# Performance work log

Measured on AMD Instinct MI355X. Metric: run time of the kernel, lower is better.

## Reference

```python
import jax, jax.numpy as jnp
import numpy as np


def setup_inputs() -> dict:
    key = jax.random.key(0)
    kq, kk, kv, kb = jax.random.split(key, 4)
    B, H, S, D = 4, 16, 1024, 64
    return {
        "query": jax.random.normal(kq, (B, H, S, D), dtype=jnp.float32),
        "key": jax.random.normal(kk, (B, H, S, D), dtype=jnp.float32),
        "value": jax.random.normal(kv, (B, H, S, D), dtype=jnp.float32),
        "bias_mask": jax.random.normal(kb, (1, 1, S, S), dtype=jnp.float32),
    }


def reference(query, key, value, bias_mask):
    d_k = query.shape[-1]
    scale = 1.0 / jnp.sqrt(jnp.asarray(d_k, dtype=query.dtype))
    # scores: [B, H, Sq, Sk]
    scores = jnp.einsum("bhqd,bhkd->bhqk", query, key) * scale
    scores = scores + bias_mask
    attn_weights = jax.nn.softmax(scores, axis=-1)
    output = jnp.einsum("bhqk,bhkd->bhqd", attn_weights, value)
    return (output, attn_weights)
```

## Files before the change

### kernel.cpp

```cpp
#include <hip/hip_runtime.h>

constexpr int SEQ = 1024;
constexpr int DH  = 64;
constexpr int QR  = 32;
constexpr int KT  = 128;
constexpr int NKT = SEQ / KT;
constexpr int KS  = 72;
constexpr int VS  = 136;
constexpr int PS  = 136;

constexpr int BUF = 26112;
constexpr int SPOFF = 17408;

typedef __bf16 bf16x8 __attribute__((ext_vector_type(8)));
typedef __bf16 bf16x4 __attribute__((ext_vector_type(4)));
typedef float  f32x4  __attribute__((ext_vector_type(4)));

__global__ __launch_bounds__(256, 2)
void attn_flash_kernel(const float* __restrict__ Q, const float* __restrict__ K,
                       const float* __restrict__ V, const float* __restrict__ bias,
                       float* __restrict__ out, float* __restrict__ attn)
{
    __shared__ __align__(16) char smem[2 * BUF];
    __shared__ __bf16 sQ[QR * KS];
    __shared__ float  sRL[2][QR];

    const int tid  = threadIdx.x;
    const int w    = tid >> 6;
    const int l    = tid & 63;
    const int qt   = w & 1;
    const int ch   = w >> 1;
    const int lm   = l & 15;
    const int lq   = l >> 4;
    const int j4   = lm & 3;
    const int m0   = lm & 12;
    const int head = blockIdx.x & 63;
    const int q0   = (blockIdx.x >> 6) * QR;
    const float scale = 0.125f;

    const float* Qh = Q + (size_t)head * SEQ * DH;
    const float* Kh = K + (size_t)head * SEQ * DH;
    const float* Vh = V + (size_t)head * SEQ * DH;
    float* outh  = out  + (size_t)head * SEQ * DH;
    float* attnh = attn + (size_t)head * SEQ * SEQ;

    const int srow = tid >> 4;
    const int sdg  = tid & 15;

    f32x4 kv[8];
    #pragma unroll
    for (int i = 0; i < 8; ++i)
        kv[i] = *(const f32x4*)(Kh + (size_t)(srow + 16 * i) * DH + sdg * 4);

    #pragma unroll
    for (int i = 0; i < 2; ++i) {
        int row = srow + 16 * i;
        f32x4 v = *(const f32x4*)(Qh + (size_t)(q0 + row) * DH + sdg * 4);
        bf16x4 b;
        b[0] = (__bf16)v[0]; b[1] = (__bf16)v[1]; b[2] = (__bf16)v[2]; b[3] = (__bf16)v[3];
        *(bf16x4*)(sQ + row * KS + sdg * 4) = b;
    }

    const int rowg = q0 + qt * 16 + lq * 4;

    f32x4 xs[NKT][4];
    float ssum[4] = {0.f, 0.f, 0.f, 0.f};

    bf16x8 aQ0, aQ1;

    #pragma unroll
    for (int kt = 0; kt < NKT; ++kt) {
        __bf16* sK = (__bf16*)(smem + (kt & 1) * BUF);
        #pragma unroll
        for (int i = 0; i < 8; ++i) {
            bf16x4 b;
            b[0] = (__bf16)kv[i][0]; b[1] = (__bf16)kv[i][1];
            b[2] = (__bf16)kv[i][2]; b[3] = (__bf16)kv[i][3];
            *(bf16x4*)(sK + (srow + 16 * i) * KS + sdg * 4) = b;
        }
        __syncthreads();

        if (kt < NKT - 1) {
            #pragma unroll
            for (int i = 0; i < 8; ++i)
                kv[i] = *(const f32x4*)(Kh + (size_t)((kt + 1) * KT + srow + 16 * i) * DH + sdg * 4);
        }
        const int colg = kt * KT + ch * 64 + lm;
        float bb[4][4];
        #pragma unroll
        for (int r = 0; r < 4; ++r) {
            const float* brow = bias + (size_t)(rowg + r) * SEQ + colg;
            bb[r][0] = brow[0]; bb[r][1] = brow[16]; bb[r][2] = brow[32]; bb[r][3] = brow[48];
        }

        if (kt == 0) {
            aQ0 = *(const bf16x8*)(sQ + (qt * 16 + lm) * KS + 0 * 32 + lq * 8);
            aQ1 = *(const bf16x8*)(sQ + (qt * 16 + lm) * KS + 1 * 32 + lq * 8);
        }

        #pragma unroll
        for (int c = 0; c < 4; ++c) xs[kt][c] = (f32x4){0.f, 0.f, 0.f, 0.f};
        __builtin_amdgcn_s_setprio(1);
        #pragma unroll
        for (int c = 0; c < 4; ++c) {
            bf16x8 bfrag = *(const bf16x8*)(sK + ((ch * 4 + c) * 16 + lm) * KS + 0 * 32 + lq * 8);
            xs[kt][c] = __builtin_amdgcn_mfma_f32_16x16x32_bf16(aQ0, bfrag, xs[kt][c], 0, 0, 0);
        }
        #pragma unroll
        for (int c = 0; c < 4; ++c) {
            bf16x8 bfrag = *(const bf16x8*)(sK + ((ch * 4 + c) * 16 + lm) * KS + 1 * 32 + lq * 8);
            xs[kt][c] = __builtin_amdgcn_mfma_f32_16x16x32_bf16(aQ1, bfrag, xs[kt][c], 0, 0, 0);
        }
        __builtin_amdgcn_s_setprio(0);

        #pragma unroll
        for (int r = 0; r < 4; ++r) {
            float e0 = __expf(xs[kt][0][r] * scale + bb[r][0]);
            float e1 = __expf(xs[kt][1][r] * scale + bb[r][1]);
            float e2 = __expf(xs[kt][2][r] * scale + bb[r][2]);
            float e3 = __expf(xs[kt][3][r] * scale + bb[r][3]);
            xs[kt][0][r] = e0; xs[kt][1][r] = e1; xs[kt][2][r] = e2; xs[kt][3][r] = e3;
            ssum[r] += (e0 + e1) + (e2 + e3);
        }
    }

    #pragma unroll
    for (int r = 0; r < 4; ++r) {
        float s = ssum[r];
        #pragma unroll
        for (int off = 1; off < 16; off <<= 1)
            s += __shfl_xor(s, off);
        ssum[r] = s;
    }
    if (lm == 0) {
        #pragma unroll
        for (int r = 0; r < 4; ++r)
            sRL[ch][qt * 16 + lq * 4 + r] = ssum[r];
    }

    const int vkb  = tid & 31;
    const int vdb0 = tid >> 5;
    f32x4 vv[2][4];
    #pragma unroll
    for (int i = 0; i < 2; ++i) {
        #pragma unroll
        for (int jj = 0; jj < 4; ++jj)
            vv[i][jj] = *(const f32x4*)(Vh + (size_t)(vkb * 4 + jj) * DH + (vdb0 + 8 * i) * 4);
    }

    __syncthreads();

    float linv[4];
    #pragma unroll
    for (int r = 0; r < 4; ++r) {
        int row = qt * 16 + lq * 4 + r;
        linv[r] = 1.0f / (sRL[0][row] + sRL[1][row]);
    }

    const int dtb = ch * 2;
    f32x4 oacc[2] = {{0,0,0,0},{0,0,0,0}};
    const bool b0 = (lm & 1) != 0;
    const bool b1 = (lm & 2) != 0;
    const int  rowt = qt * 16 + lq * 4 + j4;

    #pragma unroll
    for (int kt = 0; kt < NKT; ++kt) {
        __bf16* sV = (__bf16*)(smem + (kt & 1) * BUF);
        __bf16* sP = (__bf16*)(smem + (kt & 1) * BUF + SPOFF);

        #pragma unroll
        for (int i = 0; i < 2; ++i) {
            int k0 = vkb * 4, d0 = (vdb0 + 8 * i) * 4;
            #pragma unroll
            for (int jj = 0; jj < 4; ++jj) {
                bf16x4 b;
                b[0] = (__bf16)vv[i][0][jj]; b[1] = (__bf16)vv[i][1][jj];
                b[2] = (__bf16)vv[i][2][jj]; b[3] = (__bf16)vv[i][3][jj];
                *(bf16x4*)(sV + (d0 + jj) * VS + k0) = b;
            }
        }

        #pragma unroll
        for (int c = 0; c < 4; ++c) {
            float v0 = xs[kt][c][0] * linv[0];
            float v1 = xs[kt][c][1] * linv[1];
            float v2 = xs[kt][c][2] * linv[2];
            float v3 = xs[kt][c][3] * linv[3];
            { float a = b0 ? v0 : v1; float t = __shfl_xor(a, 1); if (b0) v0 = t; else v1 = t; }
            { float a = b0 ? v2 : v3; float t = __shfl_xor(a, 1); if (b0) v2 = t; else v3 = t; }
            { float a = b1 ? v0 : v2; float t = __shfl_xor(a, 2); if (b1) v0 = t; else v2 = t; }
            { float a = b1 ? v1 : v3; float t = __shfl_xor(a, 2); if (b1) v1 = t; else v3 = t; }
            f32x4 wv; wv[0] = v0; wv[1] = v1; wv[2] = v2; wv[3] = v3;
            float* ap = attnh + (size_t)(q0 + rowt) * SEQ + kt * KT + ch * 64 + 16 * c + m0;
            __builtin_nontemporal_store(wv, (f32x4*)ap);
            bf16x4 pb;
            pb[0] = (__bf16)v0; pb[1] = (__bf16)v1; pb[2] = (__bf16)v2; pb[3] = (__bf16)v3;
            *(bf16x4*)(sP + rowt * PS + ch * 64 + 16 * c + m0) = pb;
        }
        __syncthreads();

        if (kt < NKT - 1) {
            #pragma unroll
            for (int i = 0; i < 2; ++i) {
                #pragma unroll
                for (int jj = 0; jj < 4; ++jj)
                    vv[i][jj] = *(const f32x4*)(Vh + (size_t)((kt + 1) * KT + vkb * 4 + jj) * DH + (vdb0 + 8 * i) * 4);
            }
        }

        __builtin_amdgcn_s_setprio(1);
        #pragma unroll
        for (int ks = 0; ks < 4; ++ks) {
            bf16x8 afrag = *(const bf16x8*)(sP + (qt * 16 + lm) * PS + ks * 32 + lq * 8);
            #pragma unroll
            for (int c = 0; c < 2; ++c) {
                bf16x8 bfrag = *(const bf16x8*)(sV + ((dtb + c) * 16 + lm) * VS + ks * 32 + lq * 8);
                oacc[c] = __builtin_amdgcn_mfma_f32_16x16x32_bf16(afrag, bfrag, oacc[c], 0, 0, 0);
            }
        }
        __builtin_amdgcn_s_setprio(0);
    }

    #pragma unroll
    for (int c = 0; c < 2; ++c)
        #pragma unroll
        for (int r = 0; r < 4; ++r)
            __builtin_nontemporal_store(oacc[c][r],
                outh + (size_t)(rowg + r) * DH + (dtb + c) * 16 + lm);
}

extern "C" void kernel_launch(void* const* d_in, const int* in_sizes, int n_in,
                              void* d_out, int out_size, void* d_ws, size_t ws_size,
                              hipStream_t stream) {
    const float* Q    = (const float*)d_in[0];
    const float* K    = (const float*)d_in[1];
    const float* V    = (const float*)d_in[2];
    const float* bias = (const float*)d_in[3];
    float* out  = (float*)d_out;
    float* attn = (float*)d_out + 4 * 16 * 1024 * 64;
    dim3 grid(64 * (SEQ / QR));
    dim3 block(256);
    attn_flash_kernel<<<grid, block, 0, stream>>>(Q, K, V, bias, out, attn);
}
```

Measured before the change: 414.7 us.

## Fuse PV into the QK loop with unnormalized P and XOR-swizzled LDS

Moves the P·V MFMA into the first K-tile loop using unnormalized exponentials, and applies the 1/rowsum only to the final output. K and V tiles are now loaded together and double-buffered in LDS, and padded strides are replaced with XOR-swizzled layouts to avoid bank conflicts. The second pass now only normalizes and writes the attention weights. This removes a separate V streaming pass but adds syncs per tile and raises LDS use to about 78KB per block, which can cut occupancy.

```diff
diff --git a/kernel.cpp b/kernel.cpp
--- a/kernel.cpp
+++ b/kernel.cpp
@@ -5,35 +5,43 @@
 constexpr int QR  = 32;
 constexpr int KT  = 128;
 constexpr int NKT = SEQ / KT;
-constexpr int KS  = 72;
-constexpr int VS  = 136;
-constexpr int PS  = 136;
-
-constexpr int BUF = 26112;
-constexpr int SPOFF = 17408;
+
+constexpr int SK0 = 0;
+constexpr int SK1 = 16384;
+constexpr int SV0 = 32768;
+constexpr int SV1 = 49152;
+constexpr int SPO = 65536;
+constexpr int SQO = 73728;
+constexpr int SRL = 77824;
+constexpr int SMEM_BYTES = 78080;
 
 typedef __bf16 bf16x8 __attribute__((ext_vector_type(8)));
 typedef __bf16 bf16x4 __attribute__((ext_vector_type(4)));
 typedef float  f32x4  __attribute__((ext_vector_type(4)));
+
+__device__ __forceinline__ char* kadr(char* s, int base, int row, int colB) {
+    return s + base + row * 128 + (colB ^ ((row & 7) << 4));
+}
+__device__ __forceinline__ char* vadr(char* s, int base, int row, int colB) {
+    return s + base + row * 256 + (colB ^ ((row & 15) << 4));
+}
 
 __global__ __launch_bounds__(256, 2)
 void attn_flash_kernel(const float* __restrict__ Q, const float* __restrict__ K,
                        const float* __restrict__ V, const float* __restrict__ bias,
                        float* __restrict__ out, float* __restrict__ attn)
 {
-    __shared__ __align__(16) char smem[2 * BUF];
-    __shared__ __bf16 sQ[QR * KS];
-    __shared__ float  sRL[2][QR];
-
-    const int tid  = threadIdx.x;
-    const int w    = tid >> 6;
-    const int l    = tid & 63;
-    const int qt   = w & 1;
-    const int ch   = w >> 1;
-    const int lm   = l & 15;
-    const int lq   = l >> 4;
-    const int j4   = lm & 3;
-    const int m0   = lm & 12;
+    __shared__ __align__(16) char smem[SMEM_BYTES];
+
+    const int tid = threadIdx.x;
+    const int l   = tid & 63;
+    const int w   = tid >> 6;
+    const int qt  = w & 1;
+    const int ch  = w >> 1;
+    const int lm  = l & 15;
+    const int lq  = l >> 4;
+    const int j4  = lm & 3;
+    const int m0v = lm & 12;
     const int head = blockIdx.x & 63;
     const int q0   = (blockIdx.x >> 6) * QR;
     const float scale = 0.125f;
@@ -46,11 +54,18 @@
 
     const int srow = tid >> 4;
     const int sdg  = tid & 15;
-
-    f32x4 kv[8];
+    const int vkb  = tid & 31;
+    const int vdb0 = tid >> 5;
+
+    f32x4 kv[8], vv[2][4];
     #pragma unroll
     for (int i = 0; i < 8; ++i)
         kv[i] = *(const f32x4*)(Kh + (size_t)(srow + 16 * i) * DH + sdg * 4);
+    #pragma unroll
+    for (int i = 0; i < 2; ++i)
+        #pragma unroll
+        for (int jj = 0; jj < 4; ++jj)
+            vv[i][jj] = *(const f32x4*)(Vh + (size_t)(vkb * 4 + jj) * DH + (vdb0 + 8 * i) * 4);
 
     #pragma unroll
     for (int i = 0; i < 2; ++i) {
@@ -58,70 +73,128 @@
         f32x4 v = *(const f32x4*)(Qh + (size_t)(q0 + row) * DH + sdg * 4);
         bf16x4 b;
         b[0] = (__bf16)v[0]; b[1] = (__bf16)v[1]; b[2] = (__bf16)v[2]; b[3] = (__bf16)v[3];
-        *(bf16x4*)(sQ + row * KS + sdg * 4) = b;
-    }
-
-    const int rowg = q0 + qt * 16 + lq * 4;
+        *(bf16x4*)kadr(smem, SQO, row, sdg * 8) = b;
+    }
+    #pragma unroll
+    for (int i = 0; i < 8; ++i) {
+        bf16x4 b;
+        b[0] = (__bf16)kv[i][0]; b[1] = (__bf16)kv[i][1];
+        b[2] = (__bf16)kv[i][2]; b[3] = (__bf16)kv[i][3];
+        *(bf16x4*)kadr(smem, SK0, srow + 16 * i, sdg * 8) = b;
+    }
+    #pragma unroll
+    for (int i = 0; i < 2; ++i) {
+        int d0 = (vdb0 + 8 * i) * 4;
+        #pragma unroll
+        for (int jj = 0; jj < 4; ++jj) {
+            bf16x4 b;
+            b[0] = (__bf16)vv[i][0][jj]; b[1] = (__bf16)vv[i][1][jj];
+            b[2] = (__bf16)vv[i][2][jj]; b[3] = (__bf16)vv[i][3][jj];
+            *(bf16x4*)vadr(smem, SV0, d0 + jj, vkb * 8) = b;
+        }
+    }
+    __syncthreads();
+
+    bf16x8 aQ0 = *(const bf16x8*)kadr(smem, SQO, qt * 16 + lm, lq * 16);
+    bf16x8 aQ1 = *(const bf16x8*)kadr(smem, SQO, qt * 16 + lm, 64 + lq * 16);
 
     f32x4 xs[NKT][4];
     float ssum[4] = {0.f, 0.f, 0.f, 0.f};
-
-    bf16x8 aQ0, aQ1;
+    f32x4 oacc[2] = {{0,0,0,0},{0,0,0,0}};
+    const int dtb    = ch * 2;
+    const int rowg_l = qt * 16 + lq * 4;
 
     #pragma unroll
     for (int kt = 0; kt < NKT; ++kt) {
-        __bf16* sK = (__bf16*)(smem + (kt & 1) * BUF);
-        #pragma unroll
-        for (int i = 0; i < 8; ++i) {
-            bf16x4 b;
-            b[0] = (__bf16)kv[i][0]; b[1] = (__bf16)kv[i][1];
-            b[2] = (__bf16)kv[i][2]; b[3] = (__bf16)kv[i][3];
-            *(bf16x4*)(sK + (srow + 16 * i) * KS + sdg * 4) = b;
-        }
-        __syncthreads();
+        const int curK = (kt & 1) ? SK1 : SK0;
+        const int curV = (kt & 1) ? SV1 : SV0;
+        const int nxtK = (kt & 1) ? SK0 : SK1;
+        const int nxtV = (kt & 1) ? SV0 : SV1;
 
         if (kt < NKT - 1) {
             #pragma unroll
             for (int i = 0; i < 8; ++i)
                 kv[i] = *(const f32x4*)(Kh + (size_t)((kt + 1) * KT + srow + 16 * i) * DH + sdg * 4);
+            #pragma unroll
+            for (int i = 0; i < 2; ++i)
+                #pragma unroll
+                for (int jj = 0; jj < 4; ++jj)
+                    vv[i][jj] = *(const f32x4*)(Vh + (size_t)((kt + 1) * KT + vkb * 4 + jj) * DH + (vdb0 + 8 * i) * 4);
         }
         const int colg = kt * KT + ch * 64 + lm;
         float bb[4][4];
         #pragma unroll
         for (int r = 0; r < 4; ++r) {
-            const float* brow = bias + (size_t)(rowg + r) * SEQ + colg;
+            const float* brow = bias + (size_t)(q0 + rowg_l + r) * SEQ + colg;
             bb[r][0] = brow[0]; bb[r][1] = brow[16]; bb[r][2] = brow[32]; bb[r][3] = brow[48];
         }
 
-        if (kt == 0) {
-            aQ0 = *(const bf16x8*)(sQ + (qt * 16 + lm) * KS + 0 * 32 + lq * 8);
-            aQ1 = *(const bf16x8*)(sQ + (qt * 16 + lm) * KS + 1 * 32 + lq * 8);
-        }
-
-        #pragma unroll
-        for (int c = 0; c < 4; ++c) xs[kt][c] = (f32x4){0.f, 0.f, 0.f, 0.f};
+        f32x4 acc[4] = {{0,0,0,0},{0,0,0,0},{0,0,0,0},{0,0,0,0}};
         __builtin_amdgcn_s_setprio(1);
         #pragma unroll
         for (int c = 0; c < 4; ++c) {
-            bf16x8 bfrag = *(const bf16x8*)(sK + ((ch * 4 + c) * 16 + lm) * KS + 0 * 32 + lq * 8);
-            xs[kt][c] = __builtin_amdgcn_mfma_f32_16x16x32_bf16(aQ0, bfrag, xs[kt][c], 0, 0, 0);
+            bf16x8 bf = *(const bf16x8*)kadr(smem, curK, (ch * 4 + c) * 16 + lm, lq * 16);
+            acc[c] = __builtin_amdgcn_mfma_f32_16x16x32_bf16(aQ0, bf, acc[c], 0, 0, 0);
         }
         #pragma unroll
         for (int c = 0; c < 4; ++c) {
-            bf16x8 bfrag = *(const bf16x8*)(sK + ((ch * 4 + c) * 16 + lm) * KS + 1 * 32 + lq * 8);
-            xs[kt][c] = __builtin_amdgcn_mfma_f32_16x16x32_bf16(aQ1, bfrag, xs[kt][c], 0, 0, 0);
+            bf16x8 bf = *(const bf16x8*)kadr(smem, curK, (ch * 4 + c) * 16 + lm, 64 + lq * 16);
+            acc[c] = __builtin_amdgcn_mfma_f32_16x16x32_bf16(aQ1, bf, acc[c], 0, 0, 0);
         }
         __builtin_amdgcn_s_setprio(0);
 
         #pragma unroll
         for (int r = 0; r < 4; ++r) {
-            float e0 = __expf(xs[kt][0][r] * scale + bb[r][0]);
-            float e1 = __expf(xs[kt][1][r] * scale + bb[r][1]);
-            float e2 = __expf(xs[kt][2][r] * scale + bb[r][2]);
-            float e3 = __expf(xs[kt][3][r] * scale + bb[r][3]);
+            float e0 = __expf(acc[0][r] * scale + bb[r][0]);
+            float e1 = __expf(acc[1][r] * scale + bb[r][1]);
+            float e2 = __expf(acc[2][r] * scale + bb[r][2]);
+            float e3 = __expf(acc[3][r] * scale + bb[r][3]);
+            ssum[r] += (e0 + e1) + (e2 + e3);
             xs[kt][0][r] = e0; xs[kt][1][r] = e1; xs[kt][2][r] = e2; xs[kt][3][r] = e3;
-            ssum[r] += (e0 + e1) + (e2 + e3);
-        }
+        }
+
+        __syncthreads();
+
+        if (kt < NKT - 1) {
+            #pragma unroll
+            for (int i = 0; i < 8; ++i) {
+                bf16x4 b;
+                b[0] = (__bf16)kv[i][0]; b[1] = (__bf16)kv[i][1];
+                b[2] = (__bf16)kv[i][2]; b[3] = (__bf16)kv[i][3];
+                *(bf16x4*)kadr(smem, nxtK, srow + 16 * i, sdg * 8) = b;
+            }
+            #pragma unroll
+            for (int i = 0; i < 2; ++i) {
+                int d0 = (vdb0 + 8 * i) * 4;
+                #pragma unroll
+                for (int jj = 0; jj < 4; ++jj) {
+                    bf16x4 b;
+                    b[0] = (__bf16)vv[i][0][jj]; b[1] = (__bf16)vv[i][1][jj];
+                    b[2] = (__bf16)vv[i][2][jj]; b[3] = (__bf16)vv[i][3][jj];
+                    *(bf16x4*)vadr(smem, nxtV, d0 + jj, vkb * 8) = b;
+                }
+            }
+        }
+        #pragma unroll
+        for (int r = 0; r < 4; ++r) {
+            #pragma unroll
+            for (int c = 0; c < 4; ++c)
+                *(__bf16*)vadr(smem, SPO, rowg_l + r, ch * 128 + 32 * c + 2 * lm) =
+                    (__bf16)xs[kt][c][r];
+        }
+        __syncthreads();
+
+        __builtin_amdgcn_s_setprio(1);
+        #pragma unroll
+        for (int ks = 0; ks < 4; ++ks) {
+            bf16x8 af = *(const bf16x8*)vadr(smem, SPO, qt * 16 + lm, ks * 64 + lq * 16);
+            #pragma unroll
+            for (int c = 0; c < 2; ++c) {
+                bf16x8 bf = *(const bf16x8*)vadr(smem, curV, (dtb + c) * 16 + lm, ks * 64 + lq * 16);
+                oacc[c] = __builtin_amdgcn_mfma_f32_16x16x32_bf16(af, bf, oacc[c], 0, 0, 0);
+            }
+        }
+        __builtin_amdgcn_s_setprio(0);
     }
 
     #pragma unroll
@@ -132,54 +205,23 @@
             s += __shfl_xor(s, off);
         ssum[r] = s;
     }
+    float* sRLp = (float*)(smem + SRL);
     if (lm == 0) {
         #pragma unroll
         for (int r = 0; r < 4; ++r)
-            sRL[ch][qt * 16 + lq * 4 + r] = ssum[r];
-    }
-
-    const int vkb  = tid & 31;
-    const int vdb0 = tid >> 5;
-    f32x4 vv[2][4];
-    #pragma unroll
-    for (int i = 0; i < 2; ++i) {
-        #pragma unroll
-        for (int jj = 0; jj < 4; ++jj)
-            vv[i][jj] = *(const f32x4*)(Vh + (size_t)(vkb * 4 + jj) * DH + (vdb0 + 8 * i) * 4);
-    }
-
+            sRLp[ch * 32 + rowg_l + r] = ssum[r];
+    }
     __syncthreads();
-
     float linv[4];
     #pragma unroll
-    for (int r = 0; r < 4; ++r) {
-        int row = qt * 16 + lq * 4 + r;
-        linv[r] = 1.0f / (sRL[0][row] + sRL[1][row]);
-    }
-
-    const int dtb = ch * 2;
-    f32x4 oacc[2] = {{0,0,0,0},{0,0,0,0}};
+    for (int r = 0; r < 4; ++r)
+        linv[r] = 1.0f / (sRLp[rowg_l + r] + sRLp[32 + rowg_l + r]);
+
     const bool b0 = (lm & 1) != 0;
     const bool b1 = (lm & 2) != 0;
     const int  rowt = qt * 16 + lq * 4 + j4;
-
     #pragma unroll
     for (int kt = 0; kt < NKT; ++kt) {
-        __bf16* sV = (__bf16*)(smem + (kt & 1) * BUF);
-        __bf16* sP = (__bf16*)(smem + (kt & 1) * BUF + SPOFF);
-
-        #pragma unroll
-        for (int i = 0; i < 2; ++i) {
-            int k0 = vkb * 4, d0 = (vdb0 + 8 * i) * 4;
-            #pragma unroll
-            for (int jj = 0; jj < 4; ++jj) {
-                bf16x4 b;
-                b[0] = (__bf16)vv[i][0][jj]; b[1] = (__bf16)vv[i][1][jj];
-                b[2] = (__bf16)vv[i][2][jj]; b[3] = (__bf16)vv[i][3][jj];
-                *(bf16x4*)(sV + (d0 + jj) * VS + k0) = b;
-            }
-        }
-
         #pragma unroll
         for (int c = 0; c < 4; ++c) {
             float v0 = xs[kt][c][0] * linv[0];
@@ -191,42 +233,17 @@
             { float a = b1 ? v0 : v2; float t = __shfl_xor(a, 2); if (b1) v0 = t; else v2 = t; }
             { float a = b1 ? v1 : v3; float t = __shfl_xor(a, 2); if (b1) v1 = t; else v3 = t; }
             f32x4 wv; wv[0] = v0; wv[1] = v1; wv[2] = v2; wv[3] = v3;
-            float* ap = attnh + (size_t)(q0 + rowt) * SEQ + kt * KT + ch * 64 + 16 * c + m0;
+            float* ap = attnh + (size_t)(q0 + rowt) * SEQ + kt * KT + ch * 64 + 16 * c + m0v;
             __builtin_nontemporal_store(wv, (f32x4*)ap);
-            bf16x4 pb;
-            pb[0] = (__bf16)v0; pb[1] = (__bf16)v1; pb[2] = (__bf16)v2; pb[3] = (__bf16)v3;
-            *(bf16x4*)(sP + rowt * PS + ch * 64 + 16 * c + m0) = pb;
-        }
-        __syncthreads();
-
-        if (kt < NKT - 1) {
-            #pragma unroll
-            for (int i = 0; i < 2; ++i) {
-                #pragma unroll
-                for (int jj = 0; jj < 4; ++jj)
-                    vv[i][jj] = *(const f32x4*)(Vh + (size_t)((kt + 1) * KT + vkb * 4 + jj) * DH + (vdb0 + 8 * i) * 4);
-            }
-        }
-
-        __builtin_amdgcn_s_setprio(1);
-        #pragma unroll
-        for (int ks = 0; ks < 4; ++ks) {
-            bf16x8 afrag = *(const bf16x8*)(sP + (qt * 16 + lm) * PS + ks * 32 + lq * 8);
-            #pragma unroll
-            for (int c = 0; c < 2; ++c) {
-                bf16x8 bfrag = *(const bf16x8*)(sV + ((dtb + c) * 16 + lm) * VS + ks * 32 + lq * 8);
-                oacc[c] = __builtin_amdgcn_mfma_f32_16x16x32_bf16(afrag, bfrag, oacc[c], 0, 0, 0);
-            }
-        }
-        __builtin_amdgcn_s_setprio(0);
+        }
     }
 
     #pragma unroll
     for (int c = 0; c < 2; ++c)
         #pragma unroll
         for (int r = 0; r < 4; ++r)
-            __builtin_nontemporal_store(oacc[c][r],
-                outh + (size_t)(rowg + r) * DH + (dtb + c) * 16 + lm);
+            __builtin_nontemporal_store(oacc[c][r] * linv[r],
+                outh + (size_t)(q0 + rowg_l + r) * DH + (dtb + c) * 16 + lm);
 }
 
 extern "C" void kernel_launch(void* const* d_in, const int* in_sizes, int n_in,
```

After: 450.6 us. 8.6% more time.
